# Performance work log

Hardware: AMD Instinct MI355X
Metric: run time of the kernel (lower is better)

Reference implementation:

```python
import jax, jax.numpy as jnp
import numpy as np

B, N, CL = 128, 64, 64


def _lin_params(key, fan_in, fan_out):
    k1, k2 = jax.random.split(key)
    bound = 1.0 / np.sqrt(fan_in)
    w = jax.random.uniform(k1, (fan_in, fan_out), jnp.float32, -bound, bound)
    b = jax.random.uniform(k2, (fan_out,), jnp.float32, -bound, bound)
    return w, b


def setup_inputs() -> dict:
    key = jax.random.key(0)
    ks = jax.random.split(key, 12)
    cl = CL
    se_w1, se_b1 = _lin_params(ks[0], cl, cl)
    se_w2, se_b2 = _lin_params(ks[1], cl, cl)
    sd_w1, sd_b1 = _lin_params(ks[2], cl, 2 * cl)
    sd_w2, sd_b2 = _lin_params(ks[3], 2 * cl, 2 * cl)
    rc_w1, rc_b1 = _lin_params(ks[4], 2 * cl + 1, 2 * cl)
    rc_w2, rc_b2 = _lin_params(ks[5], 2 * cl, 2 * cl)
    rc_w3, rc_b3 = _lin_params(ks[6], 2 * cl, 2 * cl)
    an_w1, an_b1 = _lin_params(ks[7], 2 * cl + 1, cl)
    an_w2, an_b2 = _lin_params(ks[8], cl, 2 * cl)
    s = jax.random.normal(ks[9], (B, N, cl), jnp.float32)
    return dict(s=s,
                se_w1=se_w1, se_b1=se_b1, se_w2=se_w2, se_b2=se_b2,
                sd_w1=sd_w1, sd_b1=sd_b1, sd_w2=sd_w2, sd_b2=sd_b2,
                rc_w1=rc_w1, rc_b1=rc_b1, rc_w2=rc_w2, rc_b2=rc_b2,
                rc_w3=rc_w3, rc_b3=rc_b3,
                an_w1=an_w1, an_b1=an_b1, an_w2=an_w2, an_b2=an_b2)


def reference(s, se_w1, se_b1, se_w2, se_b2,
              sd_w1, sd_b1, sd_w2, sd_b2,
              rc_w1, rc_b1, rc_w2, rc_b2, rc_w3, rc_b3,
              an_w1, an_b1, an_w2, an_b2):
    relu = jax.nn.relu
    # state encoder: [B, N, cl]
    h = relu(relu(s @ se_w1 + se_b1) @ se_w2 + se_b2)
    Bn, Nn, cl = h.shape
    # all-pairs features [B, N, N, cl]
    a1 = jnp.broadcast_to(h[:, :, None, :], (Bn, Nn, Nn, cl))  # object_arg1
    a2 = jnp.broadcast_to(h[:, None, :, :], (Bn, Nn, Nn, cl))  # object_arg2
    dist = (a1[..., 0] - a2[..., 0]) ** 2 + (a1[..., 1] - a2[..., 1]) ** 2
    feat = jnp.concatenate([a1, a2, dist[..., None]], axis=-1)  # [B,N,N,2cl+1]
    rel = relu(relu(relu(feat @ rc_w1 + rc_b1) @ rc_w2 + rc_b2) @ rc_w3 + rc_b3)
    att = jax.nn.sigmoid(relu(feat @ an_w1 + an_b1) @ an_w2 + an_b2)
    rel_dyn = jnp.mean(rel * att, axis=2)  # [B, N, 2cl]
    self_dyn = relu(h @ sd_w1 + sd_b1) @ sd_w2 + sd_b2  # [B, N, 2cl]
    return jnp.mean(self_dyn + rel_dyn, axis=1)  # [B, 2cl]
```

## Files before the change

kernel.cpp:

```cpp
#include <hip/hip_runtime.h>
#include <math.h>

#define TPB 256

typedef unsigned short u16;
typedef unsigned int u32;
typedef __attribute__((ext_vector_type(8))) _Float16 f16x8;
typedef __attribute__((ext_vector_type(4))) float f32x4;

#define BLOB_U16 524288
#define BASE_RC_F32 327680
#define BASE_AN_F32 1376256
#define RC1P_F32 1900544
#define AN1P_F32 2949120
#define WS_NEED_BASES ((size_t)1900544 * 4)
#define WS_NEED_PRE   ((size_t)3473408 * 4)
#define RC1F 0
#define AN1F 16384
#define AN2F 24576
#define RC2F 40960
#define RC3F 73728

#define ENC_BLOCKS 128

__device__ __forceinline__ float h2f(u16 b) {
  return (float)__builtin_bit_cast(_Float16, b);
}
__device__ __forceinline__ u16 f2h_rne(float x) {
  return __builtin_bit_cast(u16, (_Float16)x);
}
__device__ __forceinline__ void split_f16(float x, u16& hi, u16& lo) {
  _Float16 h = (_Float16)x;
  hi = __builtin_bit_cast(u16, h);
  lo = __builtin_bit_cast(u16, (_Float16)(x - (float)h));
}
__device__ __forceinline__ unsigned pack_f16(float v0, float v1) {
  auto h = __builtin_amdgcn_cvt_pkrtz(v0, v1);
  return __builtin_bit_cast(unsigned, h);
}
__device__ __forceinline__ void split4(const float4 v, uint2& H, uint2& L) {
  _Float16 h0 = (_Float16)v.x, h1 = (_Float16)v.y;
  _Float16 h2 = (_Float16)v.z, h3 = (_Float16)v.w;
  _Float16 l0 = (_Float16)(v.x - (float)h0), l1 = (_Float16)(v.y - (float)h1);
  _Float16 l2 = (_Float16)(v.z - (float)h2), l3 = (_Float16)(v.w - (float)h3);
  H.x = (u32)__builtin_bit_cast(u16, h0) | ((u32)__builtin_bit_cast(u16, h1) << 16);
  H.y = (u32)__builtin_bit_cast(u16, h2) | ((u32)__builtin_bit_cast(u16, h3) << 16);
  L.x = (u32)__builtin_bit_cast(u16, l0) | ((u32)__builtin_bit_cast(u16, l1) << 16);
  L.y = (u32)__builtin_bit_cast(u16, l2) | ((u32)__builtin_bit_cast(u16, l3) << 16);
}
__device__ __forceinline__ void ld4(float r[4], const float* p) {
  float4 v = *(const float4*)p;
  r[0] = v.x; r[1] = v.y; r[2] = v.z; r[3] = v.w;
}

template<int KDIM, int ODIM>
__device__ __forceinline__ void prep_w(u16* __restrict__ hi, u16* __restrict__ lo,
                                       const float* __restrict__ W, int tid) {
  constexpr int N = KDIM * ODIM / TPB;
  constexpr int OSH = (ODIM == 128) ? 7 : 6;
#pragma unroll
  for (int base = 0; base < N; base += 16) {
    float v[16];
#pragma unroll
    for (int i = 0; i < 16; ++i) v[i] = W[(base + i) * TPB + tid];
#pragma unroll
    for (int i = 0; i < 16; ++i) {
      const int e = (base + i) * TPB + tid;
      const int k = e >> OSH, o = e & (ODIM - 1);
      const int idx = ((k >> 5) * (ODIM >> 4) + (o >> 4)) * 512 +
                      ((k >> 3) & 3) * 128 + (o & 15) * 8 + (k & 7);
      const float x = v[i];
      const _Float16 h = (_Float16)x;
      hi[idx] = __builtin_bit_cast(u16, h);
      lo[idx] = __builtin_bit_cast(u16, (_Float16)(x - (float)h));
    }
  }
}

template<int MT, int NCHUNK, int RSG, int TILES>
__device__ __forceinline__ void run3(f32x4 (&acc)[MT][4],
    const u16* __restrict__ wHi, const u16* __restrict__ wLo,
    const u16* __restrict__ bHi, const u16* __restrict__ bLo,
    int tg0, int quad, int l15) {
  const int lane = quad * 16 + l15;
#pragma unroll
  for (int c = 0; c < NCHUNK; ++c) {
    f16x8 Ah[MT], Al[MT];
#pragma unroll
    for (int t = 0; t < MT; ++t) {
      const int off = ((c * TILES + tg0 + t) * 64 + lane) * 8;
      Ah[t] = *(const f16x8*)(wHi + off);
      Al[t] = *(const f16x8*)(wLo + off);
    }
    const int slot = (4 * c + quad) ^ (l15 & 7);
    f16x8 Bh[4], Bl[4];
#pragma unroll
    for (int s = 0; s < 4; ++s) {
      const int off = (16 * s + l15) * (RSG * 8) + slot * 8;
      Bh[s] = *(const f16x8*)(bHi + off);
      Bl[s] = *(const f16x8*)(bLo + off);
    }
#pragma unroll
    for (int t = 0; t < MT; ++t)
#pragma unroll
      for (int s = 0; s < 4; ++s) {
        f32x4 a = acc[t][s];
        a = __builtin_amdgcn_mfma_f32_16x16x32_f16(Ah[t], Bh[s], a, 0, 0, 0);
        a = __builtin_amdgcn_mfma_f32_16x16x32_f16(Al[t], Bh[s], a, 0, 0, 0);
        a = __builtin_amdgcn_mfma_f32_16x16x32_f16(Ah[t], Bl[s], a, 0, 0, 0);
        acc[t][s] = a;
      }
  }
}

template<int MT, int RSG>
__device__ __forceinline__ void store_hl(const f32x4 (&acc)[MT][4],
    u16* __restrict__ dH, u16* __restrict__ dL, int o0, int quad, int l15) {
#pragma unroll
  for (int t = 0; t < MT; ++t) {
    const int ob = o0 + 16 * t + quad * 4;
    const int slot = (ob >> 3) ^ (l15 & 7);
    const int e = ob & 7;
#pragma unroll
    for (int s = 0; s < 4; ++s) {
      const int j = 16 * s + l15;
      float4 v = make_float4(fmaxf(acc[t][s][0], 0.f), fmaxf(acc[t][s][1], 0.f),
                             fmaxf(acc[t][s][2], 0.f), fmaxf(acc[t][s][3], 0.f));
      uint2 H, L;
      split4(v, H, L);
      *(uint2*)&dH[j * (RSG * 8) + slot * 8 + e] = H;
      *(uint2*)&dL[j * (RSG * 8) + slot * 8 + e] = L;
    }
  }
}

template<int MT>
__device__ __forceinline__ void initb(f32x4 (&acc)[MT][4], const float* bias,
                                      int o0, int quad) {
#pragma unroll
  for (int t = 0; t < MT; ++t) {
    float bb[4];
    ld4(bb, &bias[o0 + 16 * t + quad * 4]);
#pragma unroll
    for (int s = 0; s < 4; ++s) {
      f32x4 a;
#pragma unroll
      for (int r = 0; r < 4; ++r) a[r] = bb[r];
      acc[t][s] = a;
    }
  }
}
template<int MT>
__device__ __forceinline__ void zeroa(f32x4 (&acc)[MT][4]) {
#pragma unroll
  for (int t = 0; t < MT; ++t)
#pragma unroll
    for (int s = 0; s < 4; ++s) {
      f32x4 a;
#pragma unroll
      for (int r = 0; r < 4; ++r) a[r] = 0.f;
      acc[t][s] = a;
    }
}

__global__ __launch_bounds__(TPB, 1) void enc_prep_kernel(
    const float* __restrict__ s_in,
    const float* __restrict__ se_w1, const float* __restrict__ se_b1,
    const float* __restrict__ se_w2, const float* __restrict__ se_b2,
    const float* __restrict__ sd_w1, const float* __restrict__ sd_b1,
    const float* __restrict__ sd_w2, const float* __restrict__ sd_b2,
    const float* __restrict__ rc_w1, const float* __restrict__ rc_b1,
    const float* __restrict__ rc_w2, const float* __restrict__ rc_w3,
    const float* __restrict__ an_w1, const float* __restrict__ an_b1,
    const float* __restrict__ an_w2,
    u16* __restrict__ hB, u16* __restrict__ blob,
    float* __restrict__ baseRcG, float* __restrict__ baseAnG,
    float* __restrict__ rc1pG, float* __restrict__ an1pG,
    int do_bases, int do_pre,
    float* __restrict__ out) {
  if (blockIdx.x >= ENC_BLOCKS) {
    int idx = (int)(blockIdx.x - ENC_BLOCKS) * TPB + threadIdx.x;
    if (idx >= 53248) return;
    int r, base, OK, T; const float* W; int Wld, krow0, twoTerm;
    if (idx < 8192)       { r = idx;         base = RC1F; OK = 8192;  T = 8; W = rc_w1; Wld = 128; krow0 = 64; twoTerm = 1; }
    else if (idx < 12288) { r = idx - 8192;  base = AN1F; OK = 4096;  T = 4; W = an_w1; Wld = 64;  krow0 = 64; twoTerm = 1; }
    else if (idx < 20480) { r = idx - 12288; base = AN2F; OK = 8192;  T = 8; W = an_w2; Wld = 128; krow0 = 0;  twoTerm = 0; }
    else if (idx < 36864) { r = idx - 20480; base = RC2F; OK = 16384; T = 8; W = rc_w2; Wld = 128; krow0 = 0;  twoTerm = 0; }
    else                  { r = idx - 36864; base = RC3F; OK = 16384; T = 8; W = rc_w3; Wld = 128; krow0 = 0;  twoTerm = 0; }
    const int u = r & 7;
    const int lane = (r >> 3) & 63;
    const int ct = r >> 9;
    const int c = (T == 8) ? (ct >> 3) : (ct >> 2);
    const int tg = (T == 8) ? (ct & 7) : (ct & 3);
    const int o = tg * 16 + (lane & 15);
    const int k = c * 32 + (lane >> 4) * 8 + u;
    const float x = W[(krow0 + k) * Wld + o];
    if (twoTerm) {
      u16 hi, lo; split_f16(x, hi, lo);
      blob[base + r] = hi;
      blob[base + OK + r] = lo;
    } else {
      blob[base + r] = f2h_rne(x);
    }
    return;
  }

  __shared__ __align__(16) u16 sW[32768];
  __shared__ __align__(16) u16 sB0h[4096], sB0l[4096];
  __shared__ __align__(16) u16 sB1h[4096], sB1l[4096];
  __shared__ __align__(16) u16 sB2h[8192], sB2l[8192];
  __shared__ float sb[576];
  __shared__ float sRed[128];

  const int tid = threadIdx.x;
  const int w = tid >> 6, lane = tid & 63;
  const int quad = lane >> 4, l15 = lane & 15;
  const int b = blockIdx.x;
  const int o0 = w * 32;
  const int o0a = w * 16;

  if (tid < 64) {
    sb[tid] = se_b1[tid]; sb[64 + tid] = se_b2[tid]; sb[512 + tid] = an_b1[tid];
  } else if (tid < 192) {
    const int o = tid - 64;
    sb[128 + o] = sd_b1[o]; sb[256 + o] = sd_b2[o]; sb[384 + o] = rc_b1[o];
  }

  {
    const float* sp = s_in + (size_t)b * 4096;
#pragma unroll
    for (int i = 0; i < 2; ++i) {
      const int idx = tid + i * 256;
      const int j = idx >> 3, g = idx & 7;
      const float4 p0 = *(const float4*)(sp + j * 64 + g * 8);
      const float4 p1 = *(const float4*)(sp + j * 64 + g * 8 + 4);
      uint2 H0, L0, H1, L1;
      split4(p0, H0, L0);
      split4(p1, H1, L1);
      const int d = j * 64 + ((g ^ (j & 7)) * 8);
      *(uint4*)&sB0h[d] = make_uint4(H0.x, H0.y, H1.x, H1.y);
      *(uint4*)&sB0l[d] = make_uint4(L0.x, L0.y, L1.x, L1.y);
    }
  }

  prep_w<64, 64>(sW + 0, sW + 4096, se_w1, tid);
  prep_w<64, 64>(sW + 8192, sW + 12288, se_w2, tid);
  prep_w<64, 128>(sW + 16384, sW + 24576, sd_w1, tid);
  __syncthreads();

  f32x4 a64[1][4];
  f32x4 a128[2][4];

  initb<1>(a64, sb + 0, o0a, quad);
  run3<1, 2, 8, 4>(a64, sW + 0, sW + 4096, sB0h, sB0l, w, quad, l15);
  store_hl<1, 8>(a64, sB1h, sB1l, o0a, quad, l15);
  __syncthreads();

  initb<1>(a64, sb + 64, o0a, quad);
  run3<1, 2, 8, 4>(a64, sW + 8192, sW + 12288, sB1h, sB1l, w, quad, l15);
  store_hl<1, 8>(a64, sB0h, sB0l, o0a, quad, l15);
  __syncthreads();

#pragma unroll
  for (int i = 0; i < 2; ++i) {
    const int idx = tid + i * 256;
    const int j = idx >> 3, g = idx & 7;
    const uint4 v = *(const uint4*)&sB0h[j * 64 + ((g ^ (j & 7)) * 8)];
    *(uint4*)&hB[(size_t)(b * 64 + j) * 64 + g * 8] = v;
  }

  initb<2>(a128, sb + 128, o0, quad);
  run3<2, 2, 8, 8>(a128, sW + 16384, sW + 24576, sB0h, sB0l, 2 * w, quad, l15);
  store_hl<2, 16>(a128, sB2h, sB2l, o0, quad, l15);
  __syncthreads();

  prep_w<128, 128>(sW + 0, sW + 16384, sd_w2, tid);
  __syncthreads();

  zeroa<2>(a128);
  run3<2, 4, 16, 8>(a128, sW + 0, sW + 16384, sB2h, sB2l, 2 * w, quad, l15);
  {
    float ps[2][4];
#pragma unroll
    for (int t = 0; t < 2; ++t)
#pragma unroll
      for (int r = 0; r < 4; ++r) {
        float v = a128[t][0][r] + a128[t][1][r] + a128[t][2][r] + a128[t][3][r];
        v += __shfl_xor(v, 1, 64);
        v += __shfl_xor(v, 2, 64);
        v += __shfl_xor(v, 4, 64);
        v += __shfl_xor(v, 8, 64);
        ps[t][r] = v;
      }
    if (l15 == 0) {
#pragma unroll
      for (int t = 0; t < 2; ++t)
#pragma unroll
        for (int r = 0; r < 4; ++r)
          sRed[o0 + 16 * t + quad * 4 + r] = ps[t][r];
    }
  }
  __syncthreads();
  if (tid < 128)
    atomicAdd(&out[b * 128 + tid], sRed[tid] * (1.0f / 64.0f) + sb[256 + tid]);

  if (do_bases) prep_w<64, 128>(sW + 0, sW + 8192, rc_w1, tid);
  if (do_pre)   prep_w<64, 128>(sW + 16384, sW + 24576, rc_w1 + 64 * 128, tid);
  __syncthreads();

  if (do_bases) {
    initb<2>(a128, sb + 384, o0, quad);
    run3<2, 2, 8, 8>(a128, sW + 0, sW + 8192, sB0h, sB0l, 2 * w, quad, l15);
#pragma unroll
    for (int t = 0; t < 2; ++t)
#pragma unroll
      for (int s = 0; s < 4; ++s) {
        float4 v = make_float4(a128[t][s][0], a128[t][s][1], a128[t][s][2], a128[t][s][3]);
        *(float4*)&baseRcG[(size_t)(b * 64 + 16 * s + l15) * 128 + o0 + 16 * t + quad * 4] = v;
      }
  }
  if (do_pre) {
    zeroa<2>(a128);
    run3<2, 2, 8, 8>(a128, sW + 16384, sW + 24576, sB0h, sB0l, 2 * w, quad, l15);
#pragma unroll
    for (int t = 0; t < 2; ++t)
#pragma unroll
      for (int s = 0; s < 4; ++s) {
        float4 v = make_float4(a128[t][s][0], a128[t][s][1], a128[t][s][2], a128[t][s][3]);
        *(float4*)&rc1pG[(size_t)((b * 8 + 2 * w + t) * 4 + s) * 256 + lane * 4] = v;
      }
  }
  __syncthreads();

  if (do_bases) prep_w<64, 64>(sW + 0, sW + 4096, an_w1, tid);
  if (do_pre)   prep_w<64, 64>(sW + 8192, sW + 12288, an_w1 + 64 * 64, tid);
  __syncthreads();

  if (do_bases) {
    initb<1>(a64, sb + 512, o0a, quad);
    run3<1, 2, 8, 4>(a64, sW + 0, sW + 4096, sB0h, sB0l, w, quad, l15);
#pragma unroll
    for (int s = 0; s < 4; ++s) {
      float4 v = make_float4(a64[0][s][0], a64[0][s][1], a64[0][s][2], a64[0][s][3]);
      *(float4*)&baseAnG[(size_t)(b * 64 + 16 * s + l15) * 64 + o0a + quad * 4] = v;
    }
  }
  if (do_pre) {
    zeroa<1>(a64);
    run3<1, 2, 8, 4>(a64, sW + 8192, sW + 12288, sB0h, sB0l, w, quad, l15);
#pragma unroll
    for (int s = 0; s < 4; ++s) {
      float4 v = make_float4(a64[0][s][0], a64[0][s][1], a64[0][s][2], a64[0][s][3]);
      *(float4*)&an1pG[(size_t)((b * 4 + w) * 4 + s) * 256 + lane * 4] = v;
    }
  }
}

template<int MT, int NCHUNK, int RSG, int TILES>
__device__ __forceinline__ void run_layer1(f32x4 (&acc)[MT][4],
    const u16* __restrict__ blobL,
    const u16* __restrict__ sB, int tg0, int quad, int l15) {
  const int lane = quad * 16 + l15;
#pragma unroll
  for (int c = 0; c < NCHUNK; ++c) {
    f16x8 Ah[MT];
#pragma unroll
    for (int t = 0; t < MT; ++t)
      Ah[t] = *(const f16x8*)(blobL + ((c * TILES + tg0 + t) * 64 + lane) * 8);
    const int slot = (4 * c + quad) ^ (l15 & 7);
    f16x8 Bh[4];
#pragma unroll
    for (int s = 0; s < 4; ++s)
      Bh[s] = *(const f16x8*)&sB[(16 * s + l15) * (RSG * 8) + slot * 8];
#pragma unroll
    for (int t = 0; t < MT; ++t)
#pragma unroll
      for (int s = 0; s < 4; ++s)
        acc[t][s] = __builtin_amdgcn_mfma_f32_16x16x32_f16(Ah[t], Bh[s], acc[t][s], 0, 0, 0);
  }
}

template<int MT, int RSG>
__device__ __forceinline__ void store_acts_pk(const f32x4 (&acc)[MT][4],
                                              u16* dst, int o0, int quad, int l15) {
#pragma unroll
  for (int t = 0; t < MT; ++t) {
    const int ob = o0 + 16 * t + quad * 4;
    const int slot = (ob >> 3) ^ (l15 & 7);
    const int e = ob & 7;
#pragma unroll
    for (int s = 0; s < 4; ++s) {
      const int j = 16 * s + l15;
      uint2 pk;
      pk.x = pack_f16(fmaxf(acc[t][s][0], 0.f), fmaxf(acc[t][s][1], 0.f));
      pk.y = pack_f16(fmaxf(acc[t][s][2], 0.f), fmaxf(acc[t][s][3], 0.f));
      *(uint2*)&dst[j * (RSG * 8) + slot * 8 + e] = pk;
    }
  }
}

__global__ __launch_bounds__(TPB, 4) void pair_mfma_kernel(
    const u16* __restrict__ hB, const u16* __restrict__ blob,
    const float* __restrict__ baseRcG, const float* __restrict__ baseAnG,
    const float* __restrict__ rc1pG, const float* __restrict__ an1pG,
    int has_bases, int has_pre,
    const float* __restrict__ rc_w1, const float* __restrict__ rc_b1,
    const float* __restrict__ rc_b2, const float* __restrict__ rc_b3,
    const float* __restrict__ an_w1, const float* __restrict__ an_b1,
    const float* __restrict__ an_b2,
    float* __restrict__ out) {
  __shared__ __align__(16) u16 sAct[64 * 128];
  __shared__ __align__(16) u16 sAn[64 * 64];
  __shared__ float sHi[64], sDist[64];
  __shared__ float sBaseRc[128], sBaseAn[64], sW1d[128], sAnd[64];
  __shared__ float sB2[128], sB3[128], sAb2[128], sRed[128];

  const int tid = threadIdx.x;
  const int w = tid >> 6, lane = tid & 63;
  const int quad = lane >> 4, l15 = lane & 15;
  const int b = blockIdx.x >> 6, i = blockIdx.x & 63;
  const int o0 = w * 32;
  const int o0a = w * 16;

  f32x4 accR[2][4];
  f32x4 accN[1][4];

  if (has_pre) {
    if (tid < 128) {
      sW1d[tid] = rc_w1[128 * 128 + tid];
      sB2[tid] = rc_b2[tid]; sB3[tid] = rc_b3[tid]; sAb2[tid] = an_b2[tid];
    } else if (tid < 192) {
      sAnd[tid - 128] = an_w1[128 * 64 + (tid - 128)];
    } else {
      const int j = tid - 192;
      const float hi0 = h2f(hB[(b * 64 + i) * 64 + 0]);
      const float hi1 = h2f(hB[(b * 64 + i) * 64 + 1]);
      const ushort2 hj = *(const ushort2*)&hB[(b * 64 + j) * 64];
      const float d0 = hi0 - h2f(hj.x), d1 = hi1 - h2f(hj.y);
      sDist[j] = d0 * d0 + d1 * d1;
    }
    if (tid < 32)
      ((float4*)sBaseRc)[tid] = ((const float4*)(baseRcG + (size_t)(b * 64 + i) * 128))[tid];
    else if (tid < 48)
      ((float4*)sBaseAn)[tid - 32] = ((const float4*)(baseAnG + (size_t)(b * 64 + i) * 64))[tid - 32];
    __syncthreads();

    float bbR[2][4], wwR[2][4], bbN[4], wwN[4];
#pragma unroll
    for (int t = 0; t < 2; ++t) {
      ld4(bbR[t], &sBaseRc[o0 + 16 * t + quad * 4]);
      ld4(wwR[t], &sW1d[o0 + 16 * t + quad * 4]);
    }
    ld4(bbN, &sBaseAn[o0a + quad * 4]);
    ld4(wwN, &sAnd[o0a + quad * 4]);
    const float* pR = rc1pG + (size_t)(b * 8 + 2 * w) * 1024 + lane * 4;
    const float* pA = an1pG + (size_t)(b * 4 + w) * 1024 + lane * 4;
#pragma unroll
    for (int s = 0; s < 4; ++s) {
      const float dj = sDist[16 * s + l15];
#pragma unroll
      for (int t = 0; t < 2; ++t) {
        const float4 pre = *(const float4*)(pR + t * 1024 + s * 256);
        f32x4 a;
        a[0] = pre.x + fmaf(dj, wwR[t][0], bbR[t][0]);
        a[1] = pre.y + fmaf(dj, wwR[t][1], bbR[t][1]);
        a[2] = pre.z + fmaf(dj, wwR[t][2], bbR[t][2]);
        a[3] = pre.w + fmaf(dj, wwR[t][3], bbR[t][3]);
        accR[t][s] = a;
      }
      const float4 pre = *(const float4*)(pA + s * 256);
      f32x4 a;
      a[0] = pre.x + fmaf(dj, wwN[0], bbN[0]);
      a[1] = pre.y + fmaf(dj, wwN[1], bbN[1]);
      a[2] = pre.z + fmaf(dj, wwN[2], bbN[2]);
      a[3] = pre.w + fmaf(dj, wwN[3], bbN[3]);
      accN[0][s] = a;
    }
    store_acts_pk<1, 8>(accN, sAn, o0a, quad, l15);
    store_acts_pk<2, 16>(accR, sAct, o0, quad, l15);
    __syncthreads();
  } else {
    {
      const float4* srcJ = (const float4*)(hB + b * 4096);
      for (int idx = tid; idx < 512; idx += TPB) {
        const int row = idx >> 3, g = idx & 7;
        *(float4*)&sAct[row * 128 + ((g ^ (row & 7)) * 8)] = srcJ[idx];
      }
    }
    if (has_bases) {
      const float4* bR = (const float4*)(baseRcG + (size_t)(b * 64 + i) * 128);
      const float4* bA = (const float4*)(baseAnG + (size_t)(b * 64 + i) * 64);
      if (tid < 32) ((float4*)sBaseRc)[tid] = bR[tid];
      else if (tid < 48) ((float4*)sBaseAn)[tid - 32] = bA[tid - 32];
    }
    if (tid < 64) sHi[tid] = h2f(hB[(b * 64 + i) * 64 + tid]);
    if (tid < 128) {
      sW1d[tid] = rc_w1[128 * 128 + tid];
      sB2[tid] = rc_b2[tid]; sB3[tid] = rc_b3[tid]; sAb2[tid] = an_b2[tid];
    } else if (tid < 192) {
      sAnd[tid - 128] = an_w1[128 * 64 + (tid - 128)];
    }
    __syncthreads();
    if (!has_bases) {
      if (tid < 128) {
        float acc = rc_b1[tid];
        for (int k = 0; k < 64; ++k) acc = fmaf(sHi[k], rc_w1[k * 128 + tid], acc);
        sBaseRc[tid] = acc;
      } else if (tid < 192) {
        const int o = tid - 128;
        float acc = an_b1[o];
        for (int k = 0; k < 64; ++k) acc = fmaf(sHi[k], an_w1[k * 64 + o], acc);
        sBaseAn[o] = acc;
      }
    }
    if (tid >= 192) {
      const int j = tid - 192;
      const int base = j * 128 + ((0 ^ (j & 7)) * 8);
      const float d0 = sHi[0] - h2f(sAct[base + 0]);
      const float d1 = sHi[1] - h2f(sAct[base + 1]);
      sDist[j] = d0 * d0 + d1 * d1;
    }
    __syncthreads();

    {
      float bbR[2][4], wwR[2][4], bbN[4], wwN[4];
#pragma unroll
      for (int t = 0; t < 2; ++t) {
        ld4(bbR[t], &sBaseRc[o0 + 16 * t + quad * 4]);
        ld4(wwR[t], &sW1d[o0 + 16 * t + quad * 4]);
      }
      ld4(bbN, &sBaseAn[o0a + quad * 4]);
      ld4(wwN, &sAnd[o0a + quad * 4]);
#pragma unroll
      for (int s = 0; s < 4; ++s) {
        const float dj = sDist[16 * s + l15];
#pragma unroll
        for (int t = 0; t < 2; ++t) {
          f32x4 a;
#pragma unroll
          for (int r = 0; r < 4; ++r) a[r] = fmaf(dj, wwR[t][r], bbR[t][r]);
          accR[t][s] = a;
        }
        f32x4 a;
#pragma unroll
        for (int r = 0; r < 4; ++r) a[r] = fmaf(dj, wwN[r], bbN[r]);
        accN[0][s] = a;
      }
    }
    {
      const int lane64 = quad * 16 + l15;
#pragma unroll
      for (int c = 0; c < 2; ++c) {
        f16x8 Ah[2], Al[2], AhN, AlN;
#pragma unroll
        for (int t = 0; t < 2; ++t) {
          const u16* p = blob + RC1F + ((c * 8 + 2 * w + t) * 64 + lane64) * 8;
          Ah[t] = *(const f16x8*)p;
          Al[t] = *(const f16x8*)(p + 8192);
        }
        {
          const u16* p = blob + AN1F + ((c * 4 + w) * 64 + lane64) * 8;
          AhN = *(const f16x8*)p;
          AlN = *(const f16x8*)(p + 4096);
        }
        const int slot = (4 * c + quad) ^ (l15 & 7);
        f16x8 Bh[4];
#pragma unroll
        for (int s = 0; s < 4; ++s)
          Bh[s] = *(const f16x8*)&sAct[(16 * s + l15) * 128 + slot * 8];
#pragma unroll
        for (int s = 0; s < 4; ++s) {
#pragma unroll
          for (int t = 0; t < 2; ++t) {
            f32x4 a = accR[t][s];
            a = __builtin_amdgcn_mfma_f32_16x16x32_f16(Ah[t], Bh[s], a, 0, 0, 0);
            a = __builtin_amdgcn_mfma_f32_16x16x32_f16(Al[t], Bh[s], a, 0, 0, 0);
            accR[t][s] = a;
          }
          f32x4 a = accN[0][s];
          a = __builtin_amdgcn_mfma_f32_16x16x32_f16(AhN, Bh[s], a, 0, 0, 0);
          a = __builtin_amdgcn_mfma_f32_16x16x32_f16(AlN, Bh[s], a, 0, 0, 0);
          accN[0][s] = a;
        }
      }
    }
    store_acts_pk<1, 8>(accN, sAn, o0a, quad, l15);
    __syncthreads();
    store_acts_pk<2, 16>(accR, sAct, o0, quad, l15);
    __syncthreads();
  }

  {
    float bb[2][4];
#pragma unroll
    for (int t = 0; t < 2; ++t) ld4(bb[t], &sB2[o0 + 16 * t + quad * 4]);
#pragma unroll
    for (int t = 0; t < 2; ++t)
#pragma unroll
      for (int s = 0; s < 4; ++s) {
        f32x4 a;
#pragma unroll
        for (int r = 0; r < 4; ++r) a[r] = bb[t][r];
        accR[t][s] = a;
      }
  }
  run_layer1<2, 4, 16, 8>(accR, blob + RC2F, sAct, 2 * w, quad, l15);
  __syncthreads();
  store_acts_pk<2, 16>(accR, sAct, o0, quad, l15);
  __syncthreads();

  f32x4 accT[2][4];
  {
    float bb[2][4];
#pragma unroll
    for (int t = 0; t < 2; ++t) ld4(bb[t], &sAb2[o0 + 16 * t + quad * 4]);
#pragma unroll
    for (int t = 0; t < 2; ++t)
#pragma unroll
      for (int s = 0; s < 4; ++s) {
        f32x4 a;
#pragma unroll
        for (int r = 0; r < 4; ++r) a[r] = bb[t][r];
        accT[t][s] = a;
      }
  }
  run_layer1<2, 2, 8, 8>(accT, blob + AN2F, sAn, 2 * w, quad, l15);
  float att[2][4][4];
#pragma unroll
  for (int t = 0; t < 2; ++t)
#pragma unroll
    for (int s = 0; s < 4; ++s)
#pragma unroll
      for (int r = 0; r < 4; ++r)
        att[t][s][r] = __builtin_amdgcn_rcpf(1.0f + __expf(-accT[t][s][r]));

  {
    float bb[2][4];
#pragma unroll
    for (int t = 0; t < 2; ++t) ld4(bb[t], &sB3[o0 + 16 * t + quad * 4]);
#pragma unroll
    for (int t = 0; t < 2; ++t)
#pragma unroll
      for (int s = 0; s < 4; ++s) {
        f32x4 a;
#pragma unroll
        for (int r = 0; r < 4; ++r) a[r] = bb[t][r];
        accR[t][s] = a;
      }
  }
  run_layer1<2, 4, 16, 8>(accR, blob + RC3F, sAct, 2 * w, quad, l15);
  float ps[2][4] = {{0.f, 0.f, 0.f, 0.f}, {0.f, 0.f, 0.f, 0.f}};
#pragma unroll
  for (int t = 0; t < 2; ++t)
#pragma unroll
    for (int s = 0; s < 4; ++s)
#pragma unroll
      for (int r = 0; r < 4; ++r) {
        const float rel = fmaxf(accR[t][s][r], 0.f);
        ps[t][r] = fmaf(rel, att[t][s][r], ps[t][r]);
      }
#pragma unroll
  for (int t = 0; t < 2; ++t)
#pragma unroll
    for (int r = 0; r < 4; ++r) {
      float v = ps[t][r];
      v += __shfl_xor(v, 1, 64);
      v += __shfl_xor(v, 2, 64);
      v += __shfl_xor(v, 4, 64);
      v += __shfl_xor(v, 8, 64);
      ps[t][r] = v;
    }
  if (l15 == 0) {
#pragma unroll
    for (int t = 0; t < 2; ++t)
#pragma unroll
      for (int r = 0; r < 4; ++r)
        sRed[o0 + 16 * t + quad * 4 + r] = ps[t][r];
  }
  __syncthreads();
  if (tid < 128)
    atomicAdd(&out[b * 128 + tid], sRed[tid] * (1.0f / 4096.0f));
}

extern "C" void kernel_launch(void* const* d_in, const int* in_sizes, int n_in,
                              void* d_out, int out_size, void* d_ws, size_t ws_size,
                              hipStream_t stream) {
  const float* s     = (const float*)d_in[0];
  const float* se_w1 = (const float*)d_in[1];
  const float* se_b1 = (const float*)d_in[2];
  const float* se_w2 = (const float*)d_in[3];
  const float* se_b2 = (const float*)d_in[4];
  const float* sd_w1 = (const float*)d_in[5];
  const float* sd_b1 = (const float*)d_in[6];
  const float* sd_w2 = (const float*)d_in[7];
  const float* sd_b2 = (const float*)d_in[8];
  const float* rc_w1 = (const float*)d_in[9];
  const float* rc_b1 = (const float*)d_in[10];
  const float* rc_w2 = (const float*)d_in[11];
  const float* rc_b2 = (const float*)d_in[12];
  const float* rc_w3 = (const float*)d_in[13];
  const float* rc_b3 = (const float*)d_in[14];
  const float* an_w1 = (const float*)d_in[15];
  const float* an_b1 = (const float*)d_in[16];
  const float* an_w2 = (const float*)d_in[17];
  const float* an_b2 = (const float*)d_in[18];
  float* out = (float*)d_out;
  u16* hB   = (u16*)d_ws;
  u16* blob = hB + BLOB_U16;
  float* baseRcG = (float*)d_ws + BASE_RC_F32;
  float* baseAnG = (float*)d_ws + BASE_AN_F32;
  float* rc1pG   = (float*)d_ws + RC1P_F32;
  float* an1pG   = (float*)d_ws + AN1P_F32;
  const int has_pre   = (ws_size >= WS_NEED_PRE) ? 1 : 0;
  const int has_bases = (ws_size >= WS_NEED_BASES) ? 1 : 0;
  (void)n_in; (void)in_sizes;

  hipMemsetAsync(d_out, 0, (size_t)out_size * sizeof(float), stream);
  enc_prep_kernel<<<ENC_BLOCKS + 208, TPB, 0, stream>>>(s, se_w1, se_b1, se_w2, se_b2,
                                           sd_w1, sd_b1, sd_w2, sd_b2,
                                           rc_w1, rc_b1, rc_w2, rc_w3,
                                           an_w1, an_b1, an_w2,
                                           hB, blob, baseRcG, baseAnG, rc1pG, an1pG,
                                           has_bases, has_pre, out);
  pair_mfma_kernel<<<8192, TPB, 0, stream>>>(hB, blob, baseRcG, baseAnG, rc1pG, an1pG,
                                             has_bases, has_pre,
                                             rc_w1, rc_b1, rc_b2, rc_b3,
                                             an_w1, an_b1, an_b2, out);
}
```

Baseline: 180.3 us.

## Widen encoder to 512 threads, split weight prep kernel, interleave pair-kernel MFMA layers

Splits the combined encoder and weight-prep launch into two kernels. The encoder now runs with 512 threads per block, so each wave computes 16 output columns instead of 32, and only half the waves are active on the 64-wide layers. In the pair kernel, the rc layer-2 and attention layer-2 MFMA passes are issued back to back under raised wave priority, and the activation store is deferred until after the sigmoid. This is meant to shorten the serial encoder critical path and overlap more independent MFMA work, at the cost of an extra launch and possibly higher register pressure from holding both accumulator sets live.

After: 178.1 us. Within noise of the previous version (-1.2%).

```diff
diff --git a/kernel.cpp b/kernel.cpp
--- a/kernel.cpp
+++ b/kernel.cpp
@@ -2,6 +2,7 @@
 #include <math.h>
 
 #define TPB 256
+#define TPB_E 512
 
 typedef unsigned short u16;
 typedef unsigned int u32;
@@ -22,6 +23,7 @@
 #define RC3F 73728
 
 #define ENC_BLOCKS 128
+#define PREP_BLOCKS 208
 
 __device__ __forceinline__ float h2f(u16 b) {
   return (float)__builtin_bit_cast(_Float16, b);
@@ -53,19 +55,20 @@
   r[0] = v.x; r[1] = v.y; r[2] = v.z; r[3] = v.w;
 }
 
-template<int KDIM, int ODIM>
+template<int KDIM, int ODIM, int NT>
 __device__ __forceinline__ void prep_w(u16* __restrict__ hi, u16* __restrict__ lo,
                                        const float* __restrict__ W, int tid) {
-  constexpr int N = KDIM * ODIM / TPB;
+  constexpr int N = KDIM * ODIM / NT;
+  constexpr int BATCH = (N < 16) ? N : 16;
   constexpr int OSH = (ODIM == 128) ? 7 : 6;
 #pragma unroll
-  for (int base = 0; base < N; base += 16) {
-    float v[16];
-#pragma unroll
-    for (int i = 0; i < 16; ++i) v[i] = W[(base + i) * TPB + tid];
-#pragma unroll
-    for (int i = 0; i < 16; ++i) {
-      const int e = (base + i) * TPB + tid;
+  for (int base = 0; base < N; base += BATCH) {
+    float v[BATCH];
+#pragma unroll
+    for (int i = 0; i < BATCH; ++i) v[i] = W[(base + i) * NT + tid];
+#pragma unroll
+    for (int i = 0; i < BATCH; ++i) {
+      const int e = (base + i) * NT + tid;
       const int k = e >> OSH, o = e & (ODIM - 1);
       const int idx = ((k >> 5) * (ODIM >> 4) + (o >> 4)) * 512 +
                       ((k >> 3) & 3) * 128 + (o & 15) * 8 + (k & 7);
@@ -163,48 +166,19 @@
     }
 }
 
-__global__ __launch_bounds__(TPB, 1) void enc_prep_kernel(
+__global__ __launch_bounds__(TPB_E, 1) void enc_kernel(
     const float* __restrict__ s_in,
     const float* __restrict__ se_w1, const float* __restrict__ se_b1,
     const float* __restrict__ se_w2, const float* __restrict__ se_b2,
     const float* __restrict__ sd_w1, const float* __restrict__ sd_b1,
     const float* __restrict__ sd_w2, const float* __restrict__ sd_b2,
     const float* __restrict__ rc_w1, const float* __restrict__ rc_b1,
-    const float* __restrict__ rc_w2, const float* __restrict__ rc_w3,
     const float* __restrict__ an_w1, const float* __restrict__ an_b1,
-    const float* __restrict__ an_w2,
-    u16* __restrict__ hB, u16* __restrict__ blob,
+    u16* __restrict__ hB,
     float* __restrict__ baseRcG, float* __restrict__ baseAnG,
     float* __restrict__ rc1pG, float* __restrict__ an1pG,
     int do_bases, int do_pre,
     float* __restrict__ out) {
-  if (blockIdx.x >= ENC_BLOCKS) {
-    int idx = (int)(blockIdx.x - ENC_BLOCKS) * TPB + threadIdx.x;
-    if (idx >= 53248) return;
-    int r, base, OK, T; const float* W; int Wld, krow0, twoTerm;
-    if (idx < 8192)       { r = idx;         base = RC1F; OK = 8192;  T = 8; W = rc_w1; Wld = 128; krow0 = 64; twoTerm = 1; }
-    else if (idx < 12288) { r = idx - 8192;  base = AN1F; OK = 4096;  T = 4; W = an_w1; Wld = 64;  krow0 = 64; twoTerm = 1; }
-    else if (idx < 20480) { r = idx - 12288; base = AN2F; OK = 8192;  T = 8; W = an_w2; Wld = 128; krow0 = 0;  twoTerm = 0; }
-    else if (idx < 36864) { r = idx - 20480; base = RC2F; OK = 16384; T = 8; W = rc_w2; Wld = 128; krow0 = 0;  twoTerm = 0; }
-    else                  { r = idx - 36864; base = RC3F; OK = 16384; T = 8; W = rc_w3; Wld = 128; krow0 = 0;  twoTerm = 0; }
-    const int u = r & 7;
-    const int lane = (r >> 3) & 63;
-    const int ct = r >> 9;
-    const int c = (T == 8) ? (ct >> 3) : (ct >> 2);
-    const int tg = (T == 8) ? (ct & 7) : (ct & 3);
-    const int o = tg * 16 + (lane & 15);
-    const int k = c * 32 + (lane >> 4) * 8 + u;
-    const float x = W[(krow0 + k) * Wld + o];
-    if (twoTerm) {
-      u16 hi, lo; split_f16(x, hi, lo);
-      blob[base + r] = hi;
-      blob[base + OK + r] = lo;
-    } else {
-      blob[base + r] = f2h_rne(x);
-    }
-    return;
-  }
-
   __shared__ __align__(16) u16 sW[32768];
   __shared__ __align__(16) u16 sB0h[4096], sB0l[4096];
   __shared__ __align__(16) u16 sB1h[4096], sB1l[4096];
@@ -216,8 +190,8 @@
   const int w = tid >> 6, lane = tid & 63;
   const int quad = lane >> 4, l15 = lane & 15;
   const int b = blockIdx.x;
-  const int o0 = w * 32;
-  const int o0a = w * 16;
+  const int o0 = w * 16;
+  const bool act4 = (w < 4);
 
   if (tid < 64) {
     sb[tid] = se_b1[tid]; sb[64 + tid] = se_b2[tid]; sb[512 + tid] = an_b1[tid];
@@ -228,131 +202,150 @@
 
   {
     const float* sp = s_in + (size_t)b * 4096;
-#pragma unroll
-    for (int i = 0; i < 2; ++i) {
-      const int idx = tid + i * 256;
-      const int j = idx >> 3, g = idx & 7;
-      const float4 p0 = *(const float4*)(sp + j * 64 + g * 8);
-      const float4 p1 = *(const float4*)(sp + j * 64 + g * 8 + 4);
-      uint2 H0, L0, H1, L1;
-      split4(p0, H0, L0);
-      split4(p1, H1, L1);
-      const int d = j * 64 + ((g ^ (j & 7)) * 8);
-      *(uint4*)&sB0h[d] = make_uint4(H0.x, H0.y, H1.x, H1.y);
-      *(uint4*)&sB0l[d] = make_uint4(L0.x, L0.y, L1.x, L1.y);
-    }
-  }
-
-  prep_w<64, 64>(sW + 0, sW + 4096, se_w1, tid);
-  prep_w<64, 64>(sW + 8192, sW + 12288, se_w2, tid);
-  prep_w<64, 128>(sW + 16384, sW + 24576, sd_w1, tid);
-  __syncthreads();
-
-  f32x4 a64[1][4];
-  f32x4 a128[2][4];
-
-  initb<1>(a64, sb + 0, o0a, quad);
-  run3<1, 2, 8, 4>(a64, sW + 0, sW + 4096, sB0h, sB0l, w, quad, l15);
-  store_hl<1, 8>(a64, sB1h, sB1l, o0a, quad, l15);
-  __syncthreads();
-
-  initb<1>(a64, sb + 64, o0a, quad);
-  run3<1, 2, 8, 4>(a64, sW + 8192, sW + 12288, sB1h, sB1l, w, quad, l15);
-  store_hl<1, 8>(a64, sB0h, sB0l, o0a, quad, l15);
-  __syncthreads();
-
-#pragma unroll
-  for (int i = 0; i < 2; ++i) {
-    const int idx = tid + i * 256;
-    const int j = idx >> 3, g = idx & 7;
+    const int j = tid >> 3, g = tid & 7;
+    const float4 p0 = *(const float4*)(sp + j * 64 + g * 8);
+    const float4 p1 = *(const float4*)(sp + j * 64 + g * 8 + 4);
+    uint2 H0, L0, H1, L1;
+    split4(p0, H0, L0);
+    split4(p1, H1, L1);
+    const int d = j * 64 + ((g ^ (j & 7)) * 8);
+    *(uint4*)&sB0h[d] = make_uint4(H0.x, H0.y, H1.x, H1.y);
+    *(uint4*)&sB0l[d] = make_uint4(L0.x, L0.y, L1.x, L1.y);
+  }
+
+  prep_w<64, 64, TPB_E>(sW + 0, sW + 4096, se_w1, tid);
+  prep_w<64, 64, TPB_E>(sW + 8192, sW + 12288, se_w2, tid);
+  prep_w<64, 128, TPB_E>(sW + 16384, sW + 24576, sd_w1, tid);
+  __syncthreads();
+
+  f32x4 a1[1][4];
+
+  if (act4) {
+    initb<1>(a1, sb + 0, o0, quad);
+    run3<1, 2, 8, 4>(a1, sW + 0, sW + 4096, sB0h, sB0l, w, quad, l15);
+    store_hl<1, 8>(a1, sB1h, sB1l, o0, quad, l15);
+  }
+  __syncthreads();
+
+  if (act4) {
+    initb<1>(a1, sb + 64, o0, quad);
+    run3<1, 2, 8, 4>(a1, sW + 8192, sW + 12288, sB1h, sB1l, w, quad, l15);
+    store_hl<1, 8>(a1, sB0h, sB0l, o0, quad, l15);
+  }
+  __syncthreads();
+
+  {
+    const int j = tid >> 3, g = tid & 7;
     const uint4 v = *(const uint4*)&sB0h[j * 64 + ((g ^ (j & 7)) * 8)];
     *(uint4*)&hB[(size_t)(b * 64 + j) * 64 + g * 8] = v;
   }
 
-  initb<2>(a128, sb + 128, o0, quad);
-  run3<2, 2, 8, 8>(a128, sW + 16384, sW + 24576, sB0h, sB0l, 2 * w, quad, l15);
-  store_hl<2, 16>(a128, sB2h, sB2l, o0, quad, l15);
-  __syncthreads();
-
-  prep_w<128, 128>(sW + 0, sW + 16384, sd_w2, tid);
-  __syncthreads();
-
-  zeroa<2>(a128);
-  run3<2, 4, 16, 8>(a128, sW + 0, sW + 16384, sB2h, sB2l, 2 * w, quad, l15);
+  initb<1>(a1, sb + 128, o0, quad);
+  run3<1, 2, 8, 8>(a1, sW + 16384, sW + 24576, sB0h, sB0l, w, quad, l15);
+  store_hl<1, 16>(a1, sB2h, sB2l, o0, quad, l15);
+  __syncthreads();
+
+  prep_w<128, 128, TPB_E>(sW + 0, sW + 16384, sd_w2, tid);
+  __syncthreads();
+
+  zeroa<1>(a1);
+  run3<1, 4, 16, 8>(a1, sW + 0, sW + 16384, sB2h, sB2l, w, quad, l15);
   {
-    float ps[2][4];
-#pragma unroll
-    for (int t = 0; t < 2; ++t)
-#pragma unroll
-      for (int r = 0; r < 4; ++r) {
-        float v = a128[t][0][r] + a128[t][1][r] + a128[t][2][r] + a128[t][3][r];
-        v += __shfl_xor(v, 1, 64);
-        v += __shfl_xor(v, 2, 64);
-        v += __shfl_xor(v, 4, 64);
-        v += __shfl_xor(v, 8, 64);
-        ps[t][r] = v;
-      }
+    float ps[4];
+#pragma unroll
+    for (int r = 0; r < 4; ++r) {
+      float v = a1[0][0][r] + a1[0][1][r] + a1[0][2][r] + a1[0][3][r];
+      v += __shfl_xor(v, 1, 64);
+      v += __shfl_xor(v, 2, 64);
+      v += __shfl_xor(v, 4, 64);
+      v += __shfl_xor(v, 8, 64);
+      ps[r] = v;
+    }
     if (l15 == 0) {
 #pragma unroll
-      for (int t = 0; t < 2; ++t)
-#pragma unroll
-        for (int r = 0; r < 4; ++r)
-          sRed[o0 + 16 * t + quad * 4 + r] = ps[t][r];
+      for (int r = 0; r < 4; ++r) sRed[o0 + quad * 4 + r] = ps[r];
     }
   }
   __syncthreads();
   if (tid < 128)
     atomicAdd(&out[b * 128 + tid], sRed[tid] * (1.0f / 64.0f) + sb[256 + tid]);
 
-  if (do_bases) prep_w<64, 128>(sW + 0, sW + 8192, rc_w1, tid);
-  if (do_pre)   prep_w<64, 128>(sW + 16384, sW + 24576, rc_w1 + 64 * 128, tid);
+  if (do_bases) prep_w<64, 128, TPB_E>(sW + 0, sW + 8192, rc_w1, tid);
+  if (do_pre)   prep_w<64, 128, TPB_E>(sW + 16384, sW + 24576, rc_w1 + 64 * 128, tid);
   __syncthreads();
 
   if (do_bases) {
-    initb<2>(a128, sb + 384, o0, quad);
-    run3<2, 2, 8, 8>(a128, sW + 0, sW + 8192, sB0h, sB0l, 2 * w, quad, l15);
-#pragma unroll
-    for (int t = 0; t < 2; ++t)
+    initb<1>(a1, sb + 384, o0, quad);
+    run3<1, 2, 8, 8>(a1, sW + 0, sW + 8192, sB0h, sB0l, w, quad, l15);
+#pragma unroll
+    for (int s = 0; s < 4; ++s) {
+      float4 v = make_float4(a1[0][s][0], a1[0][s][1], a1[0][s][2], a1[0][s][3]);
+      *(float4*)&baseRcG[(size_t)(b * 64 + 16 * s + l15) * 128 + o0 + quad * 4] = v;
+    }
+  }
+  if (do_pre) {
+    zeroa<1>(a1);
+    run3<1, 2, 8, 8>(a1, sW + 16384, sW + 24576, sB0h, sB0l, w, quad, l15);
+#pragma unroll
+    for (int s = 0; s < 4; ++s) {
+      float4 v = make_float4(a1[0][s][0], a1[0][s][1], a1[0][s][2], a1[0][s][3]);
+      *(float4*)&rc1pG[(size_t)((b * 8 + w) * 4 + s) * 256 + lane * 4] = v;
+    }
+  }
+  __syncthreads();
+
+  if (do_bases) prep_w<64, 64, TPB_E>(sW + 0, sW + 4096, an_w1, tid);
+  if (do_pre)   prep_w<64, 64, TPB_E>(sW + 8192, sW + 12288, an_w1 + 64 * 64, tid);
+  __syncthreads();
+
+  if (act4) {
+    if (do_bases) {
+      initb<1>(a1, sb + 512, o0, quad);
+      run3<1, 2, 8, 4>(a1, sW + 0, sW + 4096, sB0h, sB0l, w, quad, l15);
 #pragma unroll
       for (int s = 0; s < 4; ++s) {
-        float4 v = make_float4(a128[t][s][0], a128[t][s][1], a128[t][s][2], a128[t][s][3]);
-        *(float4*)&baseRcG[(size_t)(b * 64 + 16 * s + l15) * 128 + o0 + 16 * t + quad * 4] = v;
-      }
-  }
-  if (do_pre) {
-    zeroa<2>(a128);
-    run3<2, 2, 8, 8>(a128, sW + 16384, sW + 24576, sB0h, sB0l, 2 * w, quad, l15);
-#pragma unroll
-    for (int t = 0; t < 2; ++t)
+        float4 v = make_float4(a1[0][s][0], a1[0][s][1], a1[0][s][2], a1[0][s][3]);
+        *(float4*)&baseAnG[(size_t)(b * 64 + 16 * s + l15) * 64 + o0 + quad * 4] = v;
+      }
+    }
+    if (do_pre) {
+      zeroa<1>(a1);
+      run3<1, 2, 8, 4>(a1, sW + 8192, sW + 12288, sB0h, sB0l, w, quad, l15);
 #pragma unroll
       for (int s = 0; s < 4; ++s) {
-        float4 v = make_float4(a128[t][s][0], a128[t][s][1], a128[t][s][2], a128[t][s][3]);
-        *(float4*)&rc1pG[(size_t)((b * 8 + 2 * w + t) * 4 + s) * 256 + lane * 4] = v;
-      }
-  }
-  __syncthreads();
-
-  if (do_bases) prep_w<64, 64>(sW + 0, sW + 4096, an_w1, tid);
-  if (do_pre)   prep_w<64, 64>(sW + 8192, sW + 12288, an_w1 + 64 * 64, tid);
-  __syncthreads();
-
-  if (do_bases) {
-    initb<1>(a64, sb + 512, o0a, quad);
-    run3<1, 2, 8, 4>(a64, sW + 0, sW + 4096, sB0h, sB0l, w, quad, l15);
-#pragma unroll
-    for (int s = 0; s < 4; ++s) {
-      float4 v = make_float4(a64[0][s][0], a64[0][s][1], a64[0][s][2], a64[0][s][3]);
-      *(float4*)&baseAnG[(size_t)(b * 64 + 16 * s + l15) * 64 + o0a + quad * 4] = v;
-    }
-  }
-  if (do_pre) {
-    zeroa<1>(a64);
-    run3<1, 2, 8, 4>(a64, sW + 8192, sW + 12288, sB0h, sB0l, w, quad, l15);
-#pragma unroll
-    for (int s = 0; s < 4; ++s) {
-      float4 v = make_float4(a64[0][s][0], a64[0][s][1], a64[0][s][2], a64[0][s][3]);
-      *(float4*)&an1pG[(size_t)((b * 4 + w) * 4 + s) * 256 + lane * 4] = v;
-    }
+        float4 v = make_float4(a1[0][s][0], a1[0][s][1], a1[0][s][2], a1[0][s][3]);
+        *(float4*)&an1pG[(size_t)((b * 4 + w) * 4 + s) * 256 + lane * 4] = v;
+      }
+    }
+  }
+}
+
+__global__ __launch_bounds__(TPB, 4) void prep_kernel(
+    const float* __restrict__ rc_w1, const float* __restrict__ rc_w2,
+    const float* __restrict__ rc_w3, const float* __restrict__ an_w1,
+    const float* __restrict__ an_w2, u16* __restrict__ blob) {
+  int idx = (int)blockIdx.x * TPB + threadIdx.x;
+  if (idx >= 53248) return;
+  int r, base, OK, T; const float* W; int Wld, krow0, twoTerm;
+  if (idx < 8192)       { r = idx;         base = RC1F; OK = 8192;  T = 8; W = rc_w1; Wld = 128; krow0 = 64; twoTerm = 1; }
+  else if (idx < 12288) { r = idx - 8192;  base = AN1F; OK = 4096;  T = 4; W = an_w1; Wld = 64;  krow0 = 64; twoTerm = 1; }
+  else if (idx < 20480) { r = idx - 12288; base = AN2F; OK = 8192;  T = 8; W = an_w2; Wld = 128; krow0 = 0;  twoTerm = 0; }
+  else if (idx < 36864) { r = idx - 20480; base = RC2F; OK = 16384; T = 8; W = rc_w2; Wld = 128; krow0 = 0;  twoTerm = 0; }
+  else                  { r = idx - 36864; base = RC3F; OK = 16384; T = 8; W = rc_w3; Wld = 128; krow0 = 0;  twoTerm = 0; }
+  const int u = r & 7;
+  const int lane = (r >> 3) & 63;
+  const int ct = r >> 9;
+  const int c = (T == 8) ? (ct >> 3) : (ct >> 2);
+  const int tg = (T == 8) ? (ct & 7) : (ct & 3);
+  const int o = tg * 16 + (lane & 15);
+  const int k = c * 32 + (lane >> 4) * 8 + u;
+  const float x = W[(krow0 + k) * Wld + o];
+  if (twoTerm) {
+    u16 hi, lo; split_f16(x, hi, lo);
+    blob[base + r] = hi;
+    blob[base + OK + r] = lo;
+  } else {
+    blob[base + r] = f2h_rne(x);
   }
 }
 
@@ -604,11 +597,6 @@
         accR[t][s] = a;
       }
   }
-  run_layer1<2, 4, 16, 8>(accR, blob + RC2F, sAct, 2 * w, quad, l15);
-  __syncthreads();
-  store_acts_pk<2, 16>(accR, sAct, o0, quad, l15);
-  __syncthreads();
-
   f32x4 accT[2][4];
   {
     float bb[2][4];
@@ -624,7 +612,10 @@
         accT[t][s] = a;
       }
   }
+  __builtin_amdgcn_s_setprio(1);
+  run_layer1<2, 4, 16, 8>(accR, blob + RC2F, sAct, 2 * w, quad, l15);
   run_layer1<2, 2, 8, 8>(accT, blob + AN2F, sAn, 2 * w, quad, l15);
+  __builtin_amdgcn_s_setprio(0);
   float att[2][4][4];
 #pragma unroll
   for (int t = 0; t < 2; ++t)
@@ -633,6 +624,9 @@
 #pragma unroll
       for (int r = 0; r < 4; ++r)
         att[t][s][r] = __builtin_amdgcn_rcpf(1.0f + __expf(-accT[t][s][r]));
+  __syncthreads();
+  store_acts_pk<2, 16>(accR, sAct, o0, quad, l15);
+  __syncthreads();
 
   {
     float bb[2][4];
@@ -648,7 +642,9 @@
         accR[t][s] = a;
       }
   }
+  __builtin_amdgcn_s_setprio(1);
   run_layer1<2, 4, 16, 8>(accR, blob + RC3F, sAct, 2 * w, quad, l15);
+  __builtin_amdgcn_s_setprio(0);
   float ps[2][4] = {{0.f, 0.f, 0.f, 0.f}, {0.f, 0.f, 0.f, 0.f}};
 #pragma unroll
   for (int t = 0; t < 2; ++t)
@@ -716,12 +712,12 @@
   (void)n_in; (void)in_sizes;
 
   hipMemsetAsync(d_out, 0, (size_t)out_size * sizeof(float), stream);
-  enc_prep_kernel<<<ENC_BLOCKS + 208, TPB, 0, stream>>>(s, se_w1, se_b1, se_w2, se_b2,
-                                           sd_w1, sd_b1, sd_w2, sd_b2,
-                                           rc_w1, rc_b1, rc_w2, rc_w3,
-                                           an_w1, an_b1, an_w2,
-                                           hB, blob, baseRcG, baseAnG, rc1pG, an1pG,
-                                           has_bases, has_pre, out);
+  enc_kernel<<<ENC_BLOCKS, TPB_E, 0, stream>>>(s, se_w1, se_b1, se_w2, se_b2,
+                                               sd_w1, sd_b1, sd_w2, sd_b2,
+                                               rc_w1, rc_b1, an_w1, an_b1,
+                                               hB, baseRcG, baseAnG, rc1pG, an1pG,
+                                               has_bases, has_pre, out);
+  prep_kernel<<<PREP_BLOCKS, TPB, 0, stream>>>(rc_w1, rc_w2, rc_w3, an_w1, an_w2, blob);
   pair_mfma_kernel<<<8192, TPB, 0, stream>>>(hB, blob, baseRcG, baseAnG, rc1pG, an1pG,
                                              has_bases, has_pre,
                                              rc_w1, rc_b1, rc_b2, rc_b3,
```
